# Kernel tuning notes

Hardware: AMD Instinct MI355X
Metric: run time of the kernel (lower is better)

## Reference

```python
import jax, jax.numpy as jnp
import numpy as np

H = 64  # hidden size
I = 300  # input size
NEG_SLOPE = 0.01  # LeakyReLU default


def _gru_scan(x_proj, W_hh, b_hh):
    """x_proj: [T, B, 3H] precomputed input projections (+ b_ih).
    Returns all hidden states [T, B, H] starting from h0 = 0."""
    B = x_proj.shape[1]
    h0 = jnp.zeros((B, H), dtype=x_proj.dtype)

    def step(h, xp):
        gh = h @ W_hh.T + b_hh  # [B, 3H]
        xr, xz, xn = jnp.split(xp, 3, axis=-1)
        hr, hz, hn = jnp.split(gh, 3, axis=-1)
        r = jax.nn.sigmoid(xr + hr)
        z = jax.nn.sigmoid(xz + hz)
        n = jnp.tanh(xn + r * hn)
        h_new = (1.0 - z) * n + z * h
        return h_new, h_new

    _, hs = jax.lax.scan(step, h0, x_proj)
    return hs  # [T, B, H]


def _forward(x, W_ih_f, W_hh_f, b_ih_f, b_hh_f, W_ih_b, W_hh_b, b_ih_b, b_hh_b,
             W1, b1, W2, b2):
    # x: [B, T, I]
    xt = jnp.swapaxes(x, 0, 1)  # [T, B, I]
    xp_f = jnp.einsum('tbi,gi->tbg', xt, W_ih_f) + b_ih_f  # [T, B, 3H]
    xp_b = jnp.einsum('tbi,gi->tbg', xt[::-1], W_ih_b) + b_ih_b

    hs_f = _gru_scan(xp_f, W_hh_f, b_hh_f)            # [T, B, H]
    hs_b = _gru_scan(xp_b, W_hh_b, b_hh_b)[::-1]      # [T, B, H] (realigned)

    out = jnp.concatenate([hs_f, hs_b], axis=-1)      # [T, B, 2H]
    x_first = out[0]    # [B, 2H]
    x_last = out[-1]    # [B, 2H]
    feat = jnp.concatenate([x_first, x_last], axis=1)  # [B, 4H]

    h1 = feat @ W1.T + b1
    h1 = jnp.where(h1 >= 0, h1, NEG_SLOPE * h1)  # LeakyReLU
    return h1 @ W2.T + b2  # [B, 1]


def setup_inputs() -> dict:
    key = jax.random.key(0)
    ks = jax.random.split(key, 16)
    B, T = 256, 512
    s_gru = 1.0 / np.sqrt(H)
    s1 = 1.0 / np.sqrt(256)
    s2 = 1.0 / np.sqrt(32)
    u = lambda k, shape, s: jax.random.uniform(k, shape, jnp.float32, -s, s)
    return {
        'x': jax.random.normal(ks[0], (B, T, I), dtype=jnp.float32),
        'W_ih_f': u(ks[1], (3 * H, I), s_gru),
        'W_hh_f': u(ks[2], (3 * H, H), s_gru),
        'b_ih_f': u(ks[3], (3 * H,), s_gru),
        'b_hh_f': u(ks[4], (3 * H,), s_gru),
        'W_ih_b': u(ks[5], (3 * H, I), s_gru),
        'W_hh_b': u(ks[6], (3 * H, H), s_gru),
        'b_ih_b': u(ks[7], (3 * H,), s_gru),
        'b_hh_b': u(ks[8], (3 * H,), s_gru),
        'W1': u(ks[9], (32, 4 * H), s1),
        'b1': u(ks[10], (32,), s1),
        'W2': u(ks[11], (1, 32), s2),
        'b2': u(ks[12], (1,), s2),
    }


def reference(x, W_ih_f, W_hh_f, b_ih_f, b_hh_f, W_ih_b, W_hh_b, b_ih_b, b_hh_b,
              W1, b1, W2, b2):
    return _forward(x, W_ih_f, W_hh_f, b_ih_f, b_hh_f,
                    W_ih_b, W_hh_b, b_ih_b, b_hh_b, W1, b1, W2, b2)
```

## Files before the change

kernel.cpp:

```cpp
#include <hip/hip_runtime.h>
#include <hip/hip_bf16.h>
#include <math.h>

#define T_LEN 512
#define B_SZ  256
#define I_SZ  300
#define H_SZ  64
#define G3    192
#define TPG   3072
#define HPAD  80

typedef float    f4v __attribute__((ext_vector_type(4)));
typedef _Float16 h4v __attribute__((ext_vector_type(4)));
typedef _Float16 h8v __attribute__((ext_vector_type(8)));

__device__ __forceinline__ float sigm_f(float x) {
    return __builtin_amdgcn_rcpf(1.f + __expf(-x));
}
__device__ __forceinline__ float tanh_f(float x) {
    float a = fabsf(x);
    float e = __expf(2.f * a);
    float t = 1.f - 2.f * __builtin_amdgcn_rcpf(1.f + e);
    return copysignf(t, x);
}

#define KC  64
#define NKC 5

__device__ __forceinline__ int stage_off(int j, int srow, int skq) {
    int g2 = (skq >> 1) & 3;
    return j * 1024 + (skq >> 3) * 512 + g2 * 128 + ((srow ^ (g2 << 1)) << 3) + (skq & 1) * 4;
}
__device__ __forceinline__ int frag_off(int tile, int kh, int lane) {
    int kgrp = lane >> 4, fr = lane & 15;
    return tile * 1024 + kh * 512 + kgrp * 128 + (((fr ^ (kgrp << 1))) << 3);
}

__global__ __launch_bounds__(256, 2) void proj_gemm(
    const float* __restrict__ x,
    const float* __restrict__ Wf, const float* __restrict__ bf,
    const float* __restrict__ Wb, const float* __restrict__ bb,
    _Float16* __restrict__ xp)
{
    __shared__ _Float16 Ap[8 * 1024];
    __shared__ _Float16 Bp[12 * 1024];

    const int tid = threadIdx.x;
    const int bid = blockIdx.x;
    const int d   = bid >> 10;
    const int G   = (bid >> 6) & 15;
    const int tc  = bid & 63;

    const float* W    = d ? Wb : Wf;
    const float* bias = d ? bb : bf;

    const int srow = tid >> 4;
    const int skq  = tid & 15;

    const int lane = tid & 63;
    const int w    = tid >> 6;
    const int wn   = (w >> 1) * 96;

    f4v acc[4][6];
    #pragma unroll
    for (int mt = 0; mt < 4; ++mt)
        #pragma unroll
        for (int nt = 0; nt < 6; ++nt) acc[mt][nt] = (f4v)0.f;

    float4 av[8], bv[12];
    {
        const bool valid = (skq * 4) <= 296;
        #pragma unroll
        for (int j = 0; j < 8; ++j)
            av[j] = valid ? *(const float4*)(x + ((size_t)(G * 16 + srow) * T_LEN + tc * 8 + j) * I_SZ + skq * 4)
                          : float4{0.f, 0.f, 0.f, 0.f};
        #pragma unroll
        for (int j = 0; j < 12; ++j)
            bv[j] = valid ? *(const float4*)(W + (size_t)(j * 16 + srow) * I_SZ + skq * 4)
                          : float4{0.f, 0.f, 0.f, 0.f};
    }

    for (int kc = 0; kc < NKC; ++kc) {
        __syncthreads();

        #pragma unroll
        for (int j = 0; j < 8; ++j) {
            h4v c = { (_Float16)av[j].x, (_Float16)av[j].y,
                      (_Float16)av[j].z, (_Float16)av[j].w };
            *(h4v*)&Ap[stage_off(j, srow, skq)] = c;
        }
        #pragma unroll
        for (int j = 0; j < 12; ++j) {
            h4v c = { (_Float16)bv[j].x, (_Float16)bv[j].y,
                      (_Float16)bv[j].z, (_Float16)bv[j].w };
            *(h4v*)&Bp[stage_off(j, srow, skq)] = c;
        }
        __syncthreads();

        if (kc + 1 < NKC) {
            const int k0 = (kc + 1) * KC;
            const bool valid = (k0 + skq * 4) <= 296;
            #pragma unroll
            for (int j = 0; j < 8; ++j)
                av[j] = valid ? *(const float4*)(x + ((size_t)(G * 16 + srow) * T_LEN + tc * 8 + j) * I_SZ + k0 + skq * 4)
                              : float4{0.f, 0.f, 0.f, 0.f};
            #pragma unroll
            for (int j = 0; j < 12; ++j)
                bv[j] = valid ? *(const float4*)(W + (size_t)(j * 16 + srow) * I_SZ + k0 + skq * 4)
                              : float4{0.f, 0.f, 0.f, 0.f};
        }

        #pragma unroll
        for (int kh = 0; kh < 2; ++kh) {
            h8v bh_[6];
            #pragma unroll
            for (int nt = 0; nt < 6; ++nt)
                bh_[nt] = *(const h8v*)&Bp[frag_off((w >> 1) * 6 + nt, kh, lane)];
            #pragma unroll
            for (int mt = 0; mt < 4; ++mt) {
                h8v ah = *(const h8v*)&Ap[frag_off((w & 1) * 4 + mt, kh, lane)];
                #pragma unroll
                for (int nt = 0; nt < 6; ++nt)
                    acc[mt][nt] = __builtin_amdgcn_mfma_f32_16x16x32_f16(ah, bh_[nt], acc[mt][nt], 0, 0, 0);
            }
        }
    }

    const int col  = lane & 15;
    const int rowq = lane >> 4;
    float bias_v[6];
    #pragma unroll
    for (int nt = 0; nt < 6; ++nt) bias_v[nt] = bias[wn + nt * 16 + col];

    _Float16* obase = xp + (size_t)(d * 16 + G) * T_LEN * TPG;
    #pragma unroll
    for (int mt = 0; mt < 4; ++mt) {
        int t = tc * 8 + (w & 1) * 4 + mt;
        _Float16* ot = obase + (size_t)t * TPG;
        #pragma unroll
        for (int nt = 0; nt < 6; ++nt) {
            int g = wn + nt * 16 + col;
            h4v c = { (_Float16)(acc[mt][nt][0] + bias_v[nt]),
                      (_Float16)(acc[mt][nt][1] + bias_v[nt]),
                      (_Float16)(acc[mt][nt][2] + bias_v[nt]),
                      (_Float16)(acc[mt][nt][3] + bias_v[nt]) };
            *(h4v*)(ot + g * 16 + rowq * 4) = c;
        }
    }
}

__global__ __launch_bounds__(256) void gru_scan(
    const _Float16* __restrict__ xp2,
    const float* __restrict__ Whf, const float* __restrict__ bhf,
    const float* __restrict__ Whb, const float* __restrict__ bhb,
    float* __restrict__ feat)
{
    const int tid  = threadIdx.x;
    const int lane = tid & 63;
    const int w    = tid >> 6;
    const int blk  = blockIdx.x;
    const int d    = blk >> 4;
    const int G    = blk & 15;
    const int col  = lane & 15;
    const int quad = lane >> 4;
    const int u    = w * 16 + col;

    const float* Whh = d ? Whb : Whf;
    const float* bhh = d ? bhb : bhf;

    h8v wb[3][2];
    f4v accb[3];
    int loff[3];
    #pragma unroll
    for (int g = 0; g < 3; ++g) {
        const int n = g * 64 + u;
        const float* wrow = Whh + (size_t)n * 64;
        #pragma unroll
        for (int c = 0; c < 2; ++c) {
            float4 w0 = *(const float4*)(wrow + c * 32 + quad * 8);
            float4 w1 = *(const float4*)(wrow + c * 32 + quad * 8 + 4);
            wb[g][c] = h8v{(_Float16)w0.x, (_Float16)w0.y, (_Float16)w0.z, (_Float16)w0.w,
                           (_Float16)w1.x, (_Float16)w1.y, (_Float16)w1.z, (_Float16)w1.w};
        }
        float bn = bhh[n];
        accb[g] = f4v{bn, bn, bn, bn};
        loff[g] = n * 16 + quad * 4;
    }

    __shared__ _Float16 hs[2][16 * HPAD];
    for (int i = tid; i < 16 * HPAD; i += 256) hs[0][i] = (_Float16)0.f;
    float hold[4] = {0.f, 0.f, 0.f, 0.f};

    const long tstep = d ? -(long)TPG : (long)TPG;
    const _Float16* base = xp2 + (size_t)(d * 16 + G) * T_LEN * TPG
                               + (size_t)(d ? T_LEN - 1 : 0) * TPG;

    h4v px[2][3];
    #pragma unroll
    for (int g = 0; g < 3; ++g) {
        px[0][g] = *(const h4v*)(base + loff[g]);
        px[1][g] = *(const h4v*)(base + tstep + loff[g]);
    }
    const _Float16* pnext = base + 2 * tstep;

    const int off_first = d ? 192 : 0;
    const int off_last  = d ? 64 : 128;

    __syncthreads();

    for (int s = 0; s < T_LEN; s += 2) {
        #pragma unroll
        for (int j = 0; j < 2; ++j) {
            const int sj = s + j;
            const _Float16* hrd = hs[j];
            _Float16*       hwr = hs[j ^ 1];

            h8v a0 = *(const h8v*)&hrd[col * HPAD + quad * 8];
            h8v a1 = *(const h8v*)&hrd[col * HPAD + 32 + quad * 8];

            f4v gh[3];
            #pragma unroll
            for (int g = 0; g < 3; ++g) {
                f4v t0 = __builtin_amdgcn_mfma_f32_16x16x32_f16(a0, wb[g][0], accb[g], 0, 0, 0);
                gh[g]  = __builtin_amdgcn_mfma_f32_16x16x32_f16(a1, wb[g][1], t0, 0, 0, 0);
            }

            h4v xc[3];
            #pragma unroll
            for (int g = 0; g < 3; ++g) xc[g] = px[j][g];
            if (sj + 2 < T_LEN) {
                #pragma unroll
                for (int g = 0; g < 3; ++g)
                    px[j][g] = *(const h4v*)(pnext + loff[g]);
                pnext += tstep;
            }

            #pragma unroll
            for (int reg = 0; reg < 4; ++reg) {
                float r = sigm_f((float)xc[0][reg] + gh[0][reg]);
                float z = sigm_f((float)xc[1][reg] + gh[1][reg]);
                float n = tanh_f((float)xc[2][reg] + r * gh[2][reg]);
                float h = fmaf(z, hold[reg] - n, n);
                hold[reg] = h;
                hwr[(quad * 4 + reg) * HPAD + u] = (_Float16)h;
            }

            if (sj == 0) {
                #pragma unroll
                for (int reg = 0; reg < 4; ++reg)
                    feat[(G * 16 + quad * 4 + reg) * 256 + off_first + u] = hold[reg];
            }
            if (sj == T_LEN - 1) {
                #pragma unroll
                for (int reg = 0; reg < 4; ++reg)
                    feat[(G * 16 + quad * 4 + reg) * 256 + off_last + u] = hold[reg];
            }
            __syncthreads();
        }
    }
}

__global__ __launch_bounds__(64) void head_k(
    const float* __restrict__ feat,
    const float* __restrict__ W1, const float* __restrict__ b1,
    const float* __restrict__ W2, const float* __restrict__ b2,
    float* __restrict__ out)
{
    __shared__ float fs[256];
    const int b = blockIdx.x;
    const int tid = threadIdx.x;
    *(float4*)&fs[tid * 4] = *(const float4*)&feat[b * 256 + tid * 4];
    __syncthreads();
    float v = 0.f;
    if (tid < 32) {
        float a = b1[tid];
        const float4* Wv = (const float4*)(W1 + tid * 256);
        const float4* fv = (const float4*)fs;
        #pragma unroll 8
        for (int k = 0; k < 64; ++k) {
            float4 wv = Wv[k], f = fv[k];
            a += wv.x * f.x + wv.y * f.y + wv.z * f.z + wv.w * f.w;
        }
        a = a >= 0.f ? a : 0.01f * a;
        v = a * W2[tid];
    }
    #pragma unroll
    for (int off = 16; off > 0; off >>= 1) v += __shfl_down(v, off);
    if (tid == 0) out[b] = v + b2[0];
}

extern "C" void kernel_launch(void* const* d_in, const int* in_sizes, int n_in,
                              void* d_out, int out_size, void* d_ws, size_t ws_size,
                              hipStream_t stream)
{
    const float* x    = (const float*)d_in[0];
    const float* Wihf = (const float*)d_in[1];
    const float* Whhf = (const float*)d_in[2];
    const float* bihf = (const float*)d_in[3];
    const float* bhhf = (const float*)d_in[4];
    const float* Wihb = (const float*)d_in[5];
    const float* Whhb = (const float*)d_in[6];
    const float* bihb = (const float*)d_in[7];
    const float* bhhb = (const float*)d_in[8];
    const float* W1   = (const float*)d_in[9];
    const float* b1   = (const float*)d_in[10];
    const float* W2   = (const float*)d_in[11];
    const float* b2   = (const float*)d_in[12];
    float* out = (float*)d_out;

    _Float16* xp2  = (_Float16*)d_ws;
    float*    feat = (float*)((char*)d_ws + (size_t)2 * B_SZ * T_LEN * G3 * 2);

    proj_gemm<<<2048, 256, 0, stream>>>(x, Wihf, bihf, Wihb, bihb, xp2);
    gru_scan<<<32, 256, 0, stream>>>(xp2, Whhf, bhhf, Whhb, bhhb, feat);
    head_k<<<256, 64, 0, stream>>>(feat, W1, b1, W2, b2, out);
}
```

Measured before the change: 570.1 us.

## Fuse projection GEMM and GRU scan with per-tile flag producer-consumer sync

Merges the input-projection GEMM and the recurrent scan into one launch. The first 32 blocks run the scans and spin on per-tile global flags, while the remaining blocks compute projection tiles in time order (reversed for the backward direction) and release a flag after each tile. This overlaps the GEMM with the latency-bound scan instead of serialising two kernels. It adds a memset, spin-waits and priority tweaks, and relies on the scan blocks being co-resident with the producer blocks, which risks stalls or deadlock if scheduling differs.

```diff
diff --git a/kernel.cpp b/kernel.cpp
--- a/kernel.cpp
+++ b/kernel.cpp
@@ -36,226 +36,256 @@
     return tile * 1024 + kh * 512 + kgrp * 128 + (((fr ^ (kgrp << 1))) << 3);
 }
 
-__global__ __launch_bounds__(256, 2) void proj_gemm(
+__device__ __forceinline__ void wait_tile(const int* flags, int idx) {
+    if (threadIdx.x == 0) {
+        if (__hip_atomic_load(&flags[idx], __ATOMIC_RELAXED, __HIP_MEMORY_SCOPE_AGENT) == 0) {
+            __builtin_amdgcn_s_setprio(0);
+            while (__hip_atomic_load(&flags[idx], __ATOMIC_RELAXED, __HIP_MEMORY_SCOPE_AGENT) == 0)
+                __builtin_amdgcn_s_sleep(8);
+            __builtin_amdgcn_s_setprio(3);
+        }
+    }
+    __syncthreads();
+    int v = __hip_atomic_load(&flags[idx], __ATOMIC_ACQUIRE, __HIP_MEMORY_SCOPE_AGENT);
+    asm volatile("" :: "v"(v));
+}
+
+__global__ __launch_bounds__(256, 2) void fused_k(
     const float* __restrict__ x,
-    const float* __restrict__ Wf, const float* __restrict__ bf,
-    const float* __restrict__ Wb, const float* __restrict__ bb,
-    _Float16* __restrict__ xp)
+    const float* __restrict__ Wihf, const float* __restrict__ bihf,
+    const float* __restrict__ Wihb, const float* __restrict__ bihb,
+    const float* __restrict__ Whhf, const float* __restrict__ bhhf,
+    const float* __restrict__ Whhb, const float* __restrict__ bhhb,
+    _Float16* __restrict__ xp, float* __restrict__ feat, int* __restrict__ flags)
 {
-    __shared__ _Float16 Ap[8 * 1024];
-    __shared__ _Float16 Bp[12 * 1024];
-
-    const int tid = threadIdx.x;
-    const int bid = blockIdx.x;
-    const int d   = bid >> 10;
-    const int G   = (bid >> 6) & 15;
-    const int tc  = bid & 63;
-
-    const float* W    = d ? Wb : Wf;
-    const float* bias = d ? bb : bf;
-
-    const int srow = tid >> 4;
-    const int skq  = tid & 15;
-
-    const int lane = tid & 63;
-    const int w    = tid >> 6;
-    const int wn   = (w >> 1) * 96;
-
-    f4v acc[4][6];
-    #pragma unroll
-    for (int mt = 0; mt < 4; ++mt)
-        #pragma unroll
-        for (int nt = 0; nt < 6; ++nt) acc[mt][nt] = (f4v)0.f;
-
-    float4 av[8], bv[12];
-    {
-        const bool valid = (skq * 4) <= 296;
-        #pragma unroll
-        for (int j = 0; j < 8; ++j)
-            av[j] = valid ? *(const float4*)(x + ((size_t)(G * 16 + srow) * T_LEN + tc * 8 + j) * I_SZ + skq * 4)
-                          : float4{0.f, 0.f, 0.f, 0.f};
-        #pragma unroll
-        for (int j = 0; j < 12; ++j)
-            bv[j] = valid ? *(const float4*)(W + (size_t)(j * 16 + srow) * I_SZ + skq * 4)
-                          : float4{0.f, 0.f, 0.f, 0.f};
-    }
-
-    for (int kc = 0; kc < NKC; ++kc) {
+    if (blockIdx.x >= 32) {
+        __shared__ _Float16 Ap[8 * 1024];
+        __shared__ _Float16 Bp[12 * 1024];
+
+        const int tid  = threadIdx.x;
+        const int pbid = blockIdx.x - 32;
+        const int kidx = pbid >> 5;
+        const int sg   = pbid & 31;
+        const int d    = sg >> 4;
+        const int G    = sg & 15;
+        const int tc   = d ? (63 - kidx) : kidx;
+
+        const float* W    = d ? Wihb : Wihf;
+        const float* bias = d ? bihb : bihf;
+
+        const int srow = tid >> 4;
+        const int skq  = tid & 15;
+
+        const int lane = tid & 63;
+        const int w    = tid >> 6;
+        const int wn   = (w >> 1) * 96;
+
+        f4v acc[4][6];
+        #pragma unroll
+        for (int mt = 0; mt < 4; ++mt)
+            #pragma unroll
+            for (int nt = 0; nt < 6; ++nt) acc[mt][nt] = (f4v)0.f;
+
+        float4 av[8], bv[12];
+        {
+            const bool valid = (skq * 4) <= 296;
+            #pragma unroll
+            for (int j = 0; j < 8; ++j)
+                av[j] = valid ? *(const float4*)(x + ((size_t)(G * 16 + srow) * T_LEN + tc * 8 + j) * I_SZ + skq * 4)
+                              : float4{0.f, 0.f, 0.f, 0.f};
+            #pragma unroll
+            for (int j = 0; j < 12; ++j)
+                bv[j] = valid ? *(const float4*)(W + (size_t)(j * 16 + srow) * I_SZ + skq * 4)
+                              : float4{0.f, 0.f, 0.f, 0.f};
+        }
+
+        for (int kc = 0; kc < NKC; ++kc) {
+            __syncthreads();
+
+            #pragma unroll
+            for (int j = 0; j < 8; ++j) {
+                h4v c = { (_Float16)av[j].x, (_Float16)av[j].y,
+                          (_Float16)av[j].z, (_Float16)av[j].w };
+                *(h4v*)&Ap[stage_off(j, srow, skq)] = c;
+            }
+            #pragma unroll
+            for (int j = 0; j < 12; ++j) {
+                h4v c = { (_Float16)bv[j].x, (_Float16)bv[j].y,
+                          (_Float16)bv[j].z, (_Float16)bv[j].w };
+                *(h4v*)&Bp[stage_off(j, srow, skq)] = c;
+            }
+            __syncthreads();
+
+            if (kc + 1 < NKC) {
+                const int k0 = (kc + 1) * KC;
+                const bool valid = (k0 + skq * 4) <= 296;
+                #pragma unroll
+                for (int j = 0; j < 8; ++j)
+                    av[j] = valid ? *(const float4*)(x + ((size_t)(G * 16 + srow) * T_LEN + tc * 8 + j) * I_SZ + k0 + skq * 4)
+                                  : float4{0.f, 0.f, 0.f, 0.f};
+                #pragma unroll
+                for (int j = 0; j < 12; ++j)
+                    bv[j] = valid ? *(const float4*)(W + (size_t)(j * 16 + srow) * I_SZ + k0 + skq * 4)
+                                  : float4{0.f, 0.f, 0.f, 0.f};
+            }
+
+            #pragma unroll
+            for (int kh = 0; kh < 2; ++kh) {
+                h8v bh_[6];
+                #pragma unroll
+                for (int nt = 0; nt < 6; ++nt)
+                    bh_[nt] = *(const h8v*)&Bp[frag_off((w >> 1) * 6 + nt, kh, lane)];
+                #pragma unroll
+                for (int mt = 0; mt < 4; ++mt) {
+                    h8v ah = *(const h8v*)&Ap[frag_off((w & 1) * 4 + mt, kh, lane)];
+                    #pragma unroll
+                    for (int nt = 0; nt < 6; ++nt)
+                        acc[mt][nt] = __builtin_amdgcn_mfma_f32_16x16x32_f16(ah, bh_[nt], acc[mt][nt], 0, 0, 0);
+                }
+            }
+        }
+
+        const int col  = lane & 15;
+        const int rowq = lane >> 4;
+        float bias_v[6];
+        #pragma unroll
+        for (int nt = 0; nt < 6; ++nt) bias_v[nt] = bias[wn + nt * 16 + col];
+
+        _Float16* obase = xp + (size_t)(d * 16 + G) * T_LEN * TPG;
+        #pragma unroll
+        for (int mt = 0; mt < 4; ++mt) {
+            int t = tc * 8 + (w & 1) * 4 + mt;
+            _Float16* ot = obase + (size_t)t * TPG;
+            #pragma unroll
+            for (int nt = 0; nt < 6; ++nt) {
+                int g = wn + nt * 16 + col;
+                h4v c = { (_Float16)(acc[mt][nt][0] + bias_v[nt]),
+                          (_Float16)(acc[mt][nt][1] + bias_v[nt]),
+                          (_Float16)(acc[mt][nt][2] + bias_v[nt]),
+                          (_Float16)(acc[mt][nt][3] + bias_v[nt]) };
+                *(h4v*)(ot + g * 16 + rowq * 4) = c;
+            }
+        }
+
         __syncthreads();
-
-        #pragma unroll
-        for (int j = 0; j < 8; ++j) {
-            h4v c = { (_Float16)av[j].x, (_Float16)av[j].y,
-                      (_Float16)av[j].z, (_Float16)av[j].w };
-            *(h4v*)&Ap[stage_off(j, srow, skq)] = c;
-        }
-        #pragma unroll
-        for (int j = 0; j < 12; ++j) {
-            h4v c = { (_Float16)bv[j].x, (_Float16)bv[j].y,
-                      (_Float16)bv[j].z, (_Float16)bv[j].w };
-            *(h4v*)&Bp[stage_off(j, srow, skq)] = c;
-        }
+        if (tid == 0)
+            __hip_atomic_store(&flags[(d * 16 + G) * 64 + tc], 1,
+                               __ATOMIC_RELEASE, __HIP_MEMORY_SCOPE_AGENT);
+    } else {
+        const int tid  = threadIdx.x;
+        const int lane = tid & 63;
+        const int w    = tid >> 6;
+        const int blk  = blockIdx.x;
+        const int d    = blk >> 4;
+        const int G    = blk & 15;
+        const int col  = lane & 15;
+        const int quad = lane >> 4;
+        const int u    = w * 16 + col;
+
+        __builtin_amdgcn_s_setprio(3);
+
+        const float* Whh = d ? Whhb : Whhf;
+        const float* bhh = d ? bhhb : bhhf;
+        const int fbase = (d * 16 + G) * 64;
+
+        h8v wb[3][2];
+        f4v accb[3];
+        int loff[3];
+        #pragma unroll
+        for (int g = 0; g < 3; ++g) {
+            const int n = g * 64 + u;
+            const float* wrow = Whh + (size_t)n * 64;
+            #pragma unroll
+            for (int c = 0; c < 2; ++c) {
+                float4 w0 = *(const float4*)(wrow + c * 32 + quad * 8);
+                float4 w1 = *(const float4*)(wrow + c * 32 + quad * 8 + 4);
+                wb[g][c] = h8v{(_Float16)w0.x, (_Float16)w0.y, (_Float16)w0.z, (_Float16)w0.w,
+                               (_Float16)w1.x, (_Float16)w1.y, (_Float16)w1.z, (_Float16)w1.w};
+            }
+            float bn = bhh[n];
+            accb[g] = f4v{bn, bn, bn, bn};
+            loff[g] = n * 16 + quad * 4;
+        }
+
+        __shared__ _Float16 hs[2][16 * HPAD];
+        for (int i = tid; i < 16 * HPAD; i += 256) hs[0][i] = (_Float16)0.f;
+        float hold[4] = {0.f, 0.f, 0.f, 0.f};
+
+        const long tstep = d ? -(long)TPG : (long)TPG;
+        const _Float16* base = xp + (size_t)(d * 16 + G) * T_LEN * TPG
+                                  + (size_t)(d ? T_LEN - 1 : 0) * TPG;
+
+        int cur_tile = d ? 63 : 0;
+        wait_tile(flags, fbase + cur_tile);
+
+        h4v px[2][3];
+        #pragma unroll
+        for (int g = 0; g < 3; ++g) {
+            px[0][g] = *(const h4v*)(base + loff[g]);
+            px[1][g] = *(const h4v*)(base + tstep + loff[g]);
+        }
+        const _Float16* pnext = base + 2 * tstep;
+
+        const int off_first = d ? 192 : 0;
+        const int off_last  = d ? 64 : 128;
+
         __syncthreads();
 
-        if (kc + 1 < NKC) {
-            const int k0 = (kc + 1) * KC;
-            const bool valid = (k0 + skq * 4) <= 296;
-            #pragma unroll
-            for (int j = 0; j < 8; ++j)
-                av[j] = valid ? *(const float4*)(x + ((size_t)(G * 16 + srow) * T_LEN + tc * 8 + j) * I_SZ + k0 + skq * 4)
-                              : float4{0.f, 0.f, 0.f, 0.f};
-            #pragma unroll
-            for (int j = 0; j < 12; ++j)
-                bv[j] = valid ? *(const float4*)(W + (size_t)(j * 16 + srow) * I_SZ + k0 + skq * 4)
-                              : float4{0.f, 0.f, 0.f, 0.f};
-        }
-
-        #pragma unroll
-        for (int kh = 0; kh < 2; ++kh) {
-            h8v bh_[6];
-            #pragma unroll
-            for (int nt = 0; nt < 6; ++nt)
-                bh_[nt] = *(const h8v*)&Bp[frag_off((w >> 1) * 6 + nt, kh, lane)];
-            #pragma unroll
-            for (int mt = 0; mt < 4; ++mt) {
-                h8v ah = *(const h8v*)&Ap[frag_off((w & 1) * 4 + mt, kh, lane)];
-                #pragma unroll
-                for (int nt = 0; nt < 6; ++nt)
-                    acc[mt][nt] = __builtin_amdgcn_mfma_f32_16x16x32_f16(ah, bh_[nt], acc[mt][nt], 0, 0, 0);
-            }
-        }
-    }
-
-    const int col  = lane & 15;
-    const int rowq = lane >> 4;
-    float bias_v[6];
-    #pragma unroll
-    for (int nt = 0; nt < 6; ++nt) bias_v[nt] = bias[wn + nt * 16 + col];
-
-    _Float16* obase = xp + (size_t)(d * 16 + G) * T_LEN * TPG;
-    #pragma unroll
-    for (int mt = 0; mt < 4; ++mt) {
-        int t = tc * 8 + (w & 1) * 4 + mt;
-        _Float16* ot = obase + (size_t)t * TPG;
-        #pragma unroll
-        for (int nt = 0; nt < 6; ++nt) {
-            int g = wn + nt * 16 + col;
-            h4v c = { (_Float16)(acc[mt][nt][0] + bias_v[nt]),
-                      (_Float16)(acc[mt][nt][1] + bias_v[nt]),
-                      (_Float16)(acc[mt][nt][2] + bias_v[nt]),
-                      (_Float16)(acc[mt][nt][3] + bias_v[nt]) };
-            *(h4v*)(ot + g * 16 + rowq * 4) = c;
-        }
-    }
-}
-
-__global__ __launch_bounds__(256) void gru_scan(
-    const _Float16* __restrict__ xp2,
-    const float* __restrict__ Whf, const float* __restrict__ bhf,
-    const float* __restrict__ Whb, const float* __restrict__ bhb,
-    float* __restrict__ feat)
-{
-    const int tid  = threadIdx.x;
-    const int lane = tid & 63;
-    const int w    = tid >> 6;
-    const int blk  = blockIdx.x;
-    const int d    = blk >> 4;
-    const int G    = blk & 15;
-    const int col  = lane & 15;
-    const int quad = lane >> 4;
-    const int u    = w * 16 + col;
-
-    const float* Whh = d ? Whb : Whf;
-    const float* bhh = d ? bhb : bhf;
-
-    h8v wb[3][2];
-    f4v accb[3];
-    int loff[3];
-    #pragma unroll
-    for (int g = 0; g < 3; ++g) {
-        const int n = g * 64 + u;
-        const float* wrow = Whh + (size_t)n * 64;
-        #pragma unroll
-        for (int c = 0; c < 2; ++c) {
-            float4 w0 = *(const float4*)(wrow + c * 32 + quad * 8);
-            float4 w1 = *(const float4*)(wrow + c * 32 + quad * 8 + 4);
-            wb[g][c] = h8v{(_Float16)w0.x, (_Float16)w0.y, (_Float16)w0.z, (_Float16)w0.w,
-                           (_Float16)w1.x, (_Float16)w1.y, (_Float16)w1.z, (_Float16)w1.w};
-        }
-        float bn = bhh[n];
-        accb[g] = f4v{bn, bn, bn, bn};
-        loff[g] = n * 16 + quad * 4;
-    }
-
-    __shared__ _Float16 hs[2][16 * HPAD];
-    for (int i = tid; i < 16 * HPAD; i += 256) hs[0][i] = (_Float16)0.f;
-    float hold[4] = {0.f, 0.f, 0.f, 0.f};
-
-    const long tstep = d ? -(long)TPG : (long)TPG;
-    const _Float16* base = xp2 + (size_t)(d * 16 + G) * T_LEN * TPG
-                               + (size_t)(d ? T_LEN - 1 : 0) * TPG;
-
-    h4v px[2][3];
-    #pragma unroll
-    for (int g = 0; g < 3; ++g) {
-        px[0][g] = *(const h4v*)(base + loff[g]);
-        px[1][g] = *(const h4v*)(base + tstep + loff[g]);
-    }
-    const _Float16* pnext = base + 2 * tstep;
-
-    const int off_first = d ? 192 : 0;
-    const int off_last  = d ? 64 : 128;
-
-    __syncthreads();
-
-    for (int s = 0; s < T_LEN; s += 2) {
-        #pragma unroll
-        for (int j = 0; j < 2; ++j) {
-            const int sj = s + j;
-            const _Float16* hrd = hs[j];
-            _Float16*       hwr = hs[j ^ 1];
-
-            h8v a0 = *(const h8v*)&hrd[col * HPAD + quad * 8];
-            h8v a1 = *(const h8v*)&hrd[col * HPAD + 32 + quad * 8];
-
-            f4v gh[3];
-            #pragma unroll
-            for (int g = 0; g < 3; ++g) {
-                f4v t0 = __builtin_amdgcn_mfma_f32_16x16x32_f16(a0, wb[g][0], accb[g], 0, 0, 0);
-                gh[g]  = __builtin_amdgcn_mfma_f32_16x16x32_f16(a1, wb[g][1], t0, 0, 0, 0);
-            }
-
-            h4v xc[3];
-            #pragma unroll
-            for (int g = 0; g < 3; ++g) xc[g] = px[j][g];
-            if (sj + 2 < T_LEN) {
-                #pragma unroll
-                for (int g = 0; g < 3; ++g)
-                    px[j][g] = *(const h4v*)(pnext + loff[g]);
-                pnext += tstep;
-            }
-
-            #pragma unroll
-            for (int reg = 0; reg < 4; ++reg) {
-                float r = sigm_f((float)xc[0][reg] + gh[0][reg]);
-                float z = sigm_f((float)xc[1][reg] + gh[1][reg]);
-                float n = tanh_f((float)xc[2][reg] + r * gh[2][reg]);
-                float h = fmaf(z, hold[reg] - n, n);
-                hold[reg] = h;
-                hwr[(quad * 4 + reg) * HPAD + u] = (_Float16)h;
-            }
-
-            if (sj == 0) {
-                #pragma unroll
-                for (int reg = 0; reg < 4; ++reg)
-                    feat[(G * 16 + quad * 4 + reg) * 256 + off_first + u] = hold[reg];
-            }
-            if (sj == T_LEN - 1) {
-                #pragma unroll
-                for (int reg = 0; reg < 4; ++reg)
-                    feat[(G * 16 + quad * 4 + reg) * 256 + off_last + u] = hold[reg];
-            }
-            __syncthreads();
+        for (int s = 0; s < T_LEN; s += 2) {
+            #pragma unroll
+            for (int j = 0; j < 2; ++j) {
+                const int sj = s + j;
+                const _Float16* hrd = hs[j];
+                _Float16*       hwr = hs[j ^ 1];
+
+                h8v a0 = *(const h8v*)&hrd[col * HPAD + quad * 8];
+                h8v a1 = *(const h8v*)&hrd[col * HPAD + 32 + quad * 8];
+
+                f4v gh[3];
+                #pragma unroll
+                for (int g = 0; g < 3; ++g) {
+                    f4v t0 = __builtin_amdgcn_mfma_f32_16x16x32_f16(a0, wb[g][0], accb[g], 0, 0, 0);
+                    gh[g]  = __builtin_amdgcn_mfma_f32_16x16x32_f16(a1, wb[g][1], t0, 0, 0, 0);
+                }
+
+                h4v xc[3];
+                #pragma unroll
+                for (int g = 0; g < 3; ++g) xc[g] = px[j][g];
+                if (sj + 2 < T_LEN) {
+                    const int mem_t = d ? (T_LEN - 3 - sj) : (sj + 2);
+                    const int tile  = mem_t >> 3;
+                    if (tile != cur_tile) {
+                        cur_tile = tile;
+                        wait_tile(flags, fbase + tile);
+                    }
+                    #pragma unroll
+                    for (int g = 0; g < 3; ++g)
+                        px[j][g] = *(const h4v*)(pnext + loff[g]);
+                    pnext += tstep;
+                }
+
+                #pragma unroll
+                for (int reg = 0; reg < 4; ++reg) {
+                    float r = sigm_f((float)xc[0][reg] + gh[0][reg]);
+                    float z = sigm_f((float)xc[1][reg] + gh[1][reg]);
+                    float n = tanh_f((float)xc[2][reg] + r * gh[2][reg]);
+                    float h = fmaf(z, hold[reg] - n, n);
+                    hold[reg] = h;
+                    hwr[(quad * 4 + reg) * HPAD + u] = (_Float16)h;
+                }
+
+                if (sj == 0) {
+                    #pragma unroll
+                    for (int reg = 0; reg < 4; ++reg)
+                        feat[(G * 16 + quad * 4 + reg) * 256 + off_first + u] = hold[reg];
+                }
+                if (sj == T_LEN - 1) {
+                    #pragma unroll
+                    for (int reg = 0; reg < 4; ++reg)
+                        feat[(G * 16 + quad * 4 + reg) * 256 + off_last + u] = hold[reg];
+                }
+                __syncthreads();
+            }
         }
     }
 }
@@ -308,10 +338,13 @@
     const float* b2   = (const float*)d_in[12];
     float* out = (float*)d_out;
 
+    const size_t xp_bytes = (size_t)2 * B_SZ * T_LEN * G3 * sizeof(_Float16);
     _Float16* xp2  = (_Float16*)d_ws;
-    float*    feat = (float*)((char*)d_ws + (size_t)2 * B_SZ * T_LEN * G3 * 2);
-
-    proj_gemm<<<2048, 256, 0, stream>>>(x, Wihf, bihf, Wihb, bihb, xp2);
-    gru_scan<<<32, 256, 0, stream>>>(xp2, Whhf, bhhf, Whhb, bhhb, feat);
+    float*    feat = (float*)((char*)d_ws + xp_bytes);
+    int*      flags = (int*)((char*)d_ws + xp_bytes + (size_t)B_SZ * 256 * sizeof(float));
+
+    hipMemsetAsync(flags, 0, 2048 * sizeof(int), stream);
+    fused_k<<<2080, 256, 0, stream>>>(x, Wihf, bihf, Wihb, bihb,
+                                      Whhf, bhhf, Whhb, bhhb, xp2, feat, flags);
     head_k<<<256, 64, 0, stream>>>(feat, W1, b1, W2, b2, out);
 }
```

Result: slower. 604.8 us (+6.1%).

## Split GRU scan across four blocks per batch group, one batch row per quad

Applied to the files above, without the earlier changes.

The recurrent scan now launches 128 blocks instead of 32, so each block handles 4 batch rows instead of 16. The MFMA is fed an A matrix built from 4 rows replicated across the 16 columns, and each lane computes the gate math for only one output element instead of four. The goal is to spread the serial recurrence over more compute units and shorten the per-step elementwise tail. In exchange most MFMA output is wasted, and the x-projection loads become scalar 16-bit reads. The __syncthreads is also replaced by a hand-written lgkmcnt wait plus s_barrier.

```diff
diff --git a/kernel.cpp b/kernel.cpp
--- a/kernel.cpp
+++ b/kernel.cpp
@@ -22,6 +22,12 @@
     float e = __expf(2.f * a);
     float t = 1.f - 2.f * __builtin_amdgcn_rcpf(1.f + e);
     return copysignf(t, x);
+}
+
+__device__ __forceinline__ void lds_barrier() {
+    __builtin_amdgcn_sched_barrier(0);
+    asm volatile("s_waitcnt lgkmcnt(0)\n\ts_barrier" ::: "memory");
+    __builtin_amdgcn_sched_barrier(0);
 }
 
 #define KC  64
@@ -159,11 +165,13 @@
     const int lane = tid & 63;
     const int w    = tid >> 6;
     const int blk  = blockIdx.x;
-    const int d    = blk >> 4;
-    const int G    = blk & 15;
+    const int d    = blk >> 6;
+    const int G    = (blk >> 2) & 15;
+    const int sub  = blk & 3;
     const int col  = lane & 15;
     const int quad = lane >> 4;
     const int u    = w * 16 + col;
+    const int bm   = sub * 4 + quad;
 
     const float* Whh = d ? Whb : Whf;
     const float* bhh = d ? bhb : bhf;
@@ -184,22 +192,22 @@
         }
         float bn = bhh[n];
         accb[g] = f4v{bn, bn, bn, bn};
-        loff[g] = n * 16 + quad * 4;
-    }
-
-    __shared__ _Float16 hs[2][16 * HPAD];
-    for (int i = tid; i < 16 * HPAD; i += 256) hs[0][i] = (_Float16)0.f;
-    float hold[4] = {0.f, 0.f, 0.f, 0.f};
+        loff[g] = n * 16 + bm;
+    }
+
+    __shared__ _Float16 hs[2][4 * HPAD];
+    for (int i = tid; i < 4 * HPAD; i += 256) hs[0][i] = (_Float16)0.f;
+    float hold = 0.f;
 
     const long tstep = d ? -(long)TPG : (long)TPG;
     const _Float16* base = xp2 + (size_t)(d * 16 + G) * T_LEN * TPG
                                + (size_t)(d ? T_LEN - 1 : 0) * TPG;
 
-    h4v px[2][3];
+    _Float16 px[2][3];
     #pragma unroll
     for (int g = 0; g < 3; ++g) {
-        px[0][g] = *(const h4v*)(base + loff[g]);
-        px[1][g] = *(const h4v*)(base + tstep + loff[g]);
+        px[0][g] = base[loff[g]];
+        px[1][g] = base[tstep + loff[g]];
     }
     const _Float16* pnext = base + 2 * tstep;
 
@@ -215,8 +223,8 @@
             const _Float16* hrd = hs[j];
             _Float16*       hwr = hs[j ^ 1];
 
-            h8v a0 = *(const h8v*)&hrd[col * HPAD + quad * 8];
-            h8v a1 = *(const h8v*)&hrd[col * HPAD + 32 + quad * 8];
+            h8v a0 = *(const h8v*)&hrd[(col >> 2) * HPAD + quad * 8];
+            h8v a1 = *(const h8v*)&hrd[(col >> 2) * HPAD + 32 + quad * 8];
 
             f4v gh[3];
             #pragma unroll
@@ -225,37 +233,29 @@
                 gh[g]  = __builtin_amdgcn_mfma_f32_16x16x32_f16(a1, wb[g][1], t0, 0, 0, 0);
             }
 
-            h4v xc[3];
-            #pragma unroll
-            for (int g = 0; g < 3; ++g) xc[g] = px[j][g];
+            _Float16 xc0 = px[j][0], xc1 = px[j][1], xc2 = px[j][2];
             if (sj + 2 < T_LEN) {
                 #pragma unroll
                 for (int g = 0; g < 3; ++g)
-                    px[j][g] = *(const h4v*)(pnext + loff[g]);
+                    px[j][g] = pnext[loff[g]];
                 pnext += tstep;
             }
 
-            #pragma unroll
-            for (int reg = 0; reg < 4; ++reg) {
-                float r = sigm_f((float)xc[0][reg] + gh[0][reg]);
-                float z = sigm_f((float)xc[1][reg] + gh[1][reg]);
-                float n = tanh_f((float)xc[2][reg] + r * gh[2][reg]);
-                float h = fmaf(z, hold[reg] - n, n);
-                hold[reg] = h;
-                hwr[(quad * 4 + reg) * HPAD + u] = (_Float16)h;
+            {
+                float r = sigm_f((float)xc0 + gh[0][0]);
+                float z = sigm_f((float)xc1 + gh[1][0]);
+                float n = tanh_f((float)xc2 + r * gh[2][0]);
+                float h = fmaf(z, hold - n, n);
+                hold = h;
+                hwr[quad * HPAD + u] = (_Float16)h;
             }
 
-            if (sj == 0) {
-                #pragma unroll
-                for (int reg = 0; reg < 4; ++reg)
-                    feat[(G * 16 + quad * 4 + reg) * 256 + off_first + u] = hold[reg];
-            }
-            if (sj == T_LEN - 1) {
-                #pragma unroll
-                for (int reg = 0; reg < 4; ++reg)
-                    feat[(G * 16 + quad * 4 + reg) * 256 + off_last + u] = hold[reg];
-            }
-            __syncthreads();
+            if (sj == 0)
+                feat[(G * 16 + bm) * 256 + off_first + u] = hold;
+            if (sj == T_LEN - 1)
+                feat[(G * 16 + bm) * 256 + off_last + u] = hold;
+
+            lds_barrier();
         }
     }
 }
@@ -312,6 +312,6 @@
     float*    feat = (float*)((char*)d_ws + (size_t)2 * B_SZ * T_LEN * G3 * 2);
 
     proj_gemm<<<2048, 256, 0, stream>>>(x, Wihf, bihf, Wihb, bihb, xp2);
-    gru_scan<<<32, 256, 0, stream>>>(xp2, Whhf, bhhf, Whhb, bhhb, feat);
+    gru_scan<<<128, 256, 0, stream>>>(xp2, Whhf, bhhf, Whhb, bhhb, feat);
     head_k<<<256, 64, 0, stream>>>(feat, W1, b1, W2, b2, out);
 }
```

Result: no change. 571.4 us (+0.2%).

## Split GRU scan into single-wave blocks of four batch rows to drop barriers

Applied to the files above, without the earlier changes.

The recurrent scan now runs 128 single-wave blocks, each owning four batch rows and all 192 gate columns, instead of 32 four-wave blocks. With one wavefront per block, the per-timestep __syncthreads is removed and hidden state is exchanged only within the wave through LDS. Each wave now issues 24 MFMAs per step with only 4 of 16 rows useful, which wastes MFMA throughput and holds more weights in registers. The projection output layout changes to row-major [t][b][g] with scalar fp16 stores, so input-gate values are read one element at a time.

```diff
diff --git a/kernel.cpp b/kernel.cpp
--- a/kernel.cpp
+++ b/kernel.cpp
@@ -8,7 +8,7 @@
 #define H_SZ  64
 #define G3    192
 #define TPG   3072
-#define HPAD  80
+#define HROW  80
 
 typedef float    f4v __attribute__((ext_vector_type(4)));
 typedef _Float16 h4v __attribute__((ext_vector_type(4)));
@@ -140,122 +140,118 @@
         #pragma unroll
         for (int nt = 0; nt < 6; ++nt) {
             int g = wn + nt * 16 + col;
-            h4v c = { (_Float16)(acc[mt][nt][0] + bias_v[nt]),
-                      (_Float16)(acc[mt][nt][1] + bias_v[nt]),
-                      (_Float16)(acc[mt][nt][2] + bias_v[nt]),
-                      (_Float16)(acc[mt][nt][3] + bias_v[nt]) };
-            *(h4v*)(ot + g * 16 + rowq * 4) = c;
-        }
-    }
-}
-
-__global__ __launch_bounds__(256) void gru_scan(
+            float bb_ = bias_v[nt];
+            #pragma unroll
+            for (int i = 0; i < 4; ++i)
+                ot[(rowq * 4 + i) * G3 + g] = (_Float16)(acc[mt][nt][i] + bb_);
+        }
+    }
+}
+
+__global__ __launch_bounds__(64, 1) void gru_scan(
     const _Float16* __restrict__ xp2,
     const float* __restrict__ Whf, const float* __restrict__ bhf,
     const float* __restrict__ Whb, const float* __restrict__ bhb,
     float* __restrict__ feat)
 {
-    const int tid  = threadIdx.x;
-    const int lane = tid & 63;
-    const int w    = tid >> 6;
+    const int lane = threadIdx.x;
     const int blk  = blockIdx.x;
-    const int d    = blk >> 4;
-    const int G    = blk & 15;
+    const int d    = blk >> 6;
+    const int G    = (blk >> 2) & 15;
+    const int sub  = blk & 3;
     const int col  = lane & 15;
     const int quad = lane >> 4;
-    const int u    = w * 16 + col;
+    const int bm   = sub * 4 + quad;
 
     const float* Whh = d ? Whb : Whf;
     const float* bhh = d ? bhb : bhf;
 
-    h8v wb[3][2];
-    f4v accb[3];
-    int loff[3];
-    #pragma unroll
-    for (int g = 0; g < 3; ++g) {
-        const int n = g * 64 + u;
+    h8v wb[12][2];
+    f4v accb[12];
+    int loff[12];
+    #pragma unroll
+    for (int ch = 0; ch < 12; ++ch) {
+        const int n = ch * 16 + col;
         const float* wrow = Whh + (size_t)n * 64;
         #pragma unroll
-        for (int c = 0; c < 2; ++c) {
-            float4 w0 = *(const float4*)(wrow + c * 32 + quad * 8);
-            float4 w1 = *(const float4*)(wrow + c * 32 + quad * 8 + 4);
-            wb[g][c] = h8v{(_Float16)w0.x, (_Float16)w0.y, (_Float16)w0.z, (_Float16)w0.w,
-                           (_Float16)w1.x, (_Float16)w1.y, (_Float16)w1.z, (_Float16)w1.w};
+        for (int kh = 0; kh < 2; ++kh) {
+            float4 w0 = *(const float4*)(wrow + kh * 32 + quad * 8);
+            float4 w1 = *(const float4*)(wrow + kh * 32 + quad * 8 + 4);
+            wb[ch][kh] = h8v{(_Float16)w0.x, (_Float16)w0.y, (_Float16)w0.z, (_Float16)w0.w,
+                             (_Float16)w1.x, (_Float16)w1.y, (_Float16)w1.z, (_Float16)w1.w};
         }
         float bn = bhh[n];
-        accb[g] = f4v{bn, bn, bn, bn};
-        loff[g] = n * 16 + quad * 4;
-    }
-
-    __shared__ _Float16 hs[2][16 * HPAD];
-    for (int i = tid; i < 16 * HPAD; i += 256) hs[0][i] = (_Float16)0.f;
+        accb[ch] = f4v{bn, bn, bn, bn};
+        loff[ch] = bm * G3 + n;
+    }
+
+    __shared__ _Float16 hb[2][4 * HROW];
+    #pragma unroll
+    for (int c = 0; c < 4; ++c) hb[0][quad * HROW + c * 16 + col] = (_Float16)0.f;
     float hold[4] = {0.f, 0.f, 0.f, 0.f};
 
     const long tstep = d ? -(long)TPG : (long)TPG;
     const _Float16* base = xp2 + (size_t)(d * 16 + G) * T_LEN * TPG
                                + (size_t)(d ? T_LEN - 1 : 0) * TPG;
 
-    h4v px[2][3];
-    #pragma unroll
-    for (int g = 0; g < 3; ++g) {
-        px[0][g] = *(const h4v*)(base + loff[g]);
-        px[1][g] = *(const h4v*)(base + tstep + loff[g]);
+    _Float16 px[2][12];
+    #pragma unroll
+    for (int ch = 0; ch < 12; ++ch) {
+        px[0][ch] = base[loff[ch]];
+        px[1][ch] = base[tstep + loff[ch]];
     }
     const _Float16* pnext = base + 2 * tstep;
 
     const int off_first = d ? 192 : 0;
     const int off_last  = d ? 64 : 128;
 
-    __syncthreads();
-
     for (int s = 0; s < T_LEN; s += 2) {
         #pragma unroll
         for (int j = 0; j < 2; ++j) {
             const int sj = s + j;
-            const _Float16* hrd = hs[j];
-            _Float16*       hwr = hs[j ^ 1];
-
-            h8v a0 = *(const h8v*)&hrd[col * HPAD + quad * 8];
-            h8v a1 = *(const h8v*)&hrd[col * HPAD + 32 + quad * 8];
-
-            f4v gh[3];
-            #pragma unroll
-            for (int g = 0; g < 3; ++g) {
-                f4v t0 = __builtin_amdgcn_mfma_f32_16x16x32_f16(a0, wb[g][0], accb[g], 0, 0, 0);
-                gh[g]  = __builtin_amdgcn_mfma_f32_16x16x32_f16(a1, wb[g][1], t0, 0, 0, 0);
-            }
-
-            h4v xc[3];
-            #pragma unroll
-            for (int g = 0; g < 3; ++g) xc[g] = px[j][g];
+            const _Float16* hr = hb[j];
+            _Float16*       hw = hb[j ^ 1];
+
+            h8v a0 = *(const h8v*)&hr[(col >> 2) * HROW + quad * 8];
+            h8v a1 = *(const h8v*)&hr[(col >> 2) * HROW + 32 + quad * 8];
+
+            f4v gh[12];
+            #pragma unroll
+            for (int ch = 0; ch < 12; ++ch) {
+                f4v t0 = __builtin_amdgcn_mfma_f32_16x16x32_f16(a0, wb[ch][0], accb[ch], 0, 0, 0);
+                gh[ch] = __builtin_amdgcn_mfma_f32_16x16x32_f16(a1, wb[ch][1], t0, 0, 0, 0);
+            }
+
+            _Float16 xc[12];
+            #pragma unroll
+            for (int ch = 0; ch < 12; ++ch) xc[ch] = px[j][ch];
             if (sj + 2 < T_LEN) {
                 #pragma unroll
-                for (int g = 0; g < 3; ++g)
-                    px[j][g] = *(const h4v*)(pnext + loff[g]);
+                for (int ch = 0; ch < 12; ++ch)
+                    px[j][ch] = pnext[loff[ch]];
                 pnext += tstep;
             }
 
             #pragma unroll
-            for (int reg = 0; reg < 4; ++reg) {
-                float r = sigm_f((float)xc[0][reg] + gh[0][reg]);
-                float z = sigm_f((float)xc[1][reg] + gh[1][reg]);
-                float n = tanh_f((float)xc[2][reg] + r * gh[2][reg]);
-                float h = fmaf(z, hold[reg] - n, n);
-                hold[reg] = h;
-                hwr[(quad * 4 + reg) * HPAD + u] = (_Float16)h;
+            for (int c = 0; c < 4; ++c) {
+                float r = sigm_f((float)xc[c]     + gh[c][0]);
+                float z = sigm_f((float)xc[4 + c] + gh[4 + c][0]);
+                float n = tanh_f((float)xc[8 + c] + r * gh[8 + c][0]);
+                float h = fmaf(z, hold[c] - n, n);
+                hold[c] = h;
+                hw[quad * HROW + c * 16 + col] = (_Float16)h;
             }
 
             if (sj == 0) {
                 #pragma unroll
-                for (int reg = 0; reg < 4; ++reg)
-                    feat[(G * 16 + quad * 4 + reg) * 256 + off_first + u] = hold[reg];
+                for (int c = 0; c < 4; ++c)
+                    feat[(G * 16 + bm) * 256 + off_first + c * 16 + col] = hold[c];
             }
             if (sj == T_LEN - 1) {
                 #pragma unroll
-                for (int reg = 0; reg < 4; ++reg)
-                    feat[(G * 16 + quad * 4 + reg) * 256 + off_last + u] = hold[reg];
-            }
-            __syncthreads();
+                for (int c = 0; c < 4; ++c)
+                    feat[(G * 16 + bm) * 256 + off_last + c * 16 + col] = hold[c];
+            }
         }
     }
 }
@@ -312,6 +308,6 @@
     float*    feat = (float*)((char*)d_ws + (size_t)2 * B_SZ * T_LEN * G3 * 2);
 
     proj_gemm<<<2048, 256, 0, stream>>>(x, Wihf, bihf, Wihb, bihb, xp2);
-    gru_scan<<<32, 256, 0, stream>>>(xp2, Whhf, bhhf, Whhb, bhhb, feat);
+    gru_scan<<<128, 64, 0, stream>>>(xp2, Whhf, bhhf, Whhb, bhhb, feat);
     head_k<<<256, 64, 0, stream>>>(feat, W1, b1, W2, b2, out);
 }
```

Measured after the change: 721.3 us. 1.27x slower.
